# Kernel optimization log

Hardware: AMD Instinct MI355X
Metric: run time of the kernel (lower is better)

The kernel has to match this reference:

```python
import jax, jax.numpy as jnp
import numpy as np

B, C, H, W = 32, 64, 56, 56
REPN, NK, SMALL = 50, 17, 3   # repN=64-int(64*0.23), nk=ceil(51/3)
GROUPS = 4                     # N_rep
EPS = 1e-5


def _build_index_mats():
    """Reduce the fallback's python scatter-add loops to exact linear maps.
    For flat position p=r*NK+j the roll shifts depend only on p%3, so each
    shift class s gets a (REPN,NK) count matrix over source nk-slots."""
    rng = np.random.RandomState(123)
    ghost = np.sort(rng.choice(C, C - REPN, replace=False))
    rep = np.array(sorted(set(range(C)) - set(ghost.tolist())), np.int32)
    Mh = np.zeros((3, REPN, NK), np.int32)
    Mv = np.zeros((3, REPN, NK), np.int32)
    Mid = np.zeros((REPN, NK), np.int32)
    for _ in range(GROUPS):
        for r in range(REPN):
            perm = rng.permutation(NK)
            for p in range(NK):
                Mh[(r * NK + p) % 3, r, perm[p]] += 1
        for r in range(REPN):
            perm = rng.permutation(NK)
            for p in range(NK):
                Mv[(r * NK + p) % 3, r, perm[p]] += 1
        kk = rng.randint(0, NK, REPN)
        for r in range(REPN):
            Mid[r, kk[r]] += 1
    return ghost.astype(np.int32), rep, Mh, Mv, Mid


def setup_inputs() -> dict:
    key = jax.random.key(0)
    k1, k2, k3 = jax.random.split(key, 3)
    ghost, rep, Mh, Mv, Mid = _build_index_mats()
    return {
        "inputs": jax.random.normal(k1, (B, C, H, W), jnp.float32),
        "w0": jax.random.normal(k2, (REPN * NK, 1, SMALL, SMALL), jnp.float32) * 0.1,
        "w1": jax.random.normal(k3, (REPN * NK, 1, SMALL, SMALL), jnp.float32) * 0.1,
        "Mh": jnp.asarray(Mh), "Mv": jnp.asarray(Mv), "Mid": jnp.asarray(Mid),
        "ghost_idx": jnp.asarray(ghost), "rep_idx": jnp.asarray(rep),
    }


def _bn(x):
    # BatchNorm2d in training mode, affine weight=1 / bias=0 (init values)
    m = x.mean(axis=(0, 2, 3), keepdims=True)
    v = x.var(axis=(0, 2, 3), keepdims=True)
    return (x - m) / jnp.sqrt(v + EPS)


def reference(inputs, w0, w1, Mh, Mv, Mid, ghost_idx, rep_idx):
    rep_in = inputs[:, rep_idx]      # (B, REPN, H, W)
    ghost_in = inputs[:, ghost_idx]  # (B, ghostN, H, W)

    def conv(w):  # depthwise-grouped conv: groups=REPN, each 1->NK channels
        return jax.lax.conv_general_dilated(
            rep_in, w, window_strides=(1, 1), padding=((2, 2), (2, 2)),
            dimension_numbers=('NCHW', 'OIHW', 'NCHW'),
            feature_group_count=REPN)

    out = conv(w0) + conv(w1)                       # (B, REPN*NK, H+2, W+2)
    xv = out.reshape(B, REPN, NK, H + 2, W + 2)

    Mhf, Mvf, Midf = (m.astype(xv.dtype) for m in (Mh, Mv, Mid))
    sh1, sw1 = (0, 1, 2), (0, 2, 1)   # lora1: shifts (i%3, 2i%3)
    sh2, sw2 = (0, 2, 1), (0, 1, 2)   # lora2: shifts (2i%3, i%3)

    lora1 = sum(jnp.roll(jnp.einsum('rk,brkhw->brhw', Mhf[s], xv),
                         (sh1[s], sw1[s]), axis=(2, 3)) for s in range(3))
    lora2 = sum(jnp.roll(jnp.einsum('rk,brkhw->brhw', Mvf[s], xv),
                         (sh2[s], sw2[s]), axis=(2, 3)) for s in range(3))
    small = jnp.einsum('rk,brkhw->brhw', Midf, xv)

    # center-crop back to (H, W): dh = dw = 1
    lora1 = lora1[:, :, 1:1 + H, 1:1 + W]
    lora2 = lora2[:, :, 1:1 + H, 1:1 + W]
    small = small[:, :, 1:1 + H, 1:1 + W]

    x = _bn(lora1) + _bn(lora2) + _bn(small) + rep_in
    return jnp.concatenate([x, ghost_in], axis=1)   # (B, C, H, W)
```

## Files before the change

kernel.cpp:

```cpp
#include <hip/hip_runtime.h>
#include <hip/hip_cooperative_groups.h>

namespace cg = cooperative_groups;

#define Bn 32
#define Cn 64
#define Hn 56
#define Wn 56
#define REPN 50
#define NKn 17
#define HWn (Hn*Wn)
#define NSTATf 100352.0f
#define EPSf 1e-5f

#define PART_OFF 0
#define WEFF_OFF 9600
#define WEFF_N   (REPN*72)

#define SEGH 7
#define NTASK 112
#define GRID_FUSED 2048

__device__ __forceinline__ void weff_one(int idx,
        const float* __restrict__ w0, const float* __restrict__ w1,
        const int* __restrict__ Mh, const int* __restrict__ Mv,
        const int* __restrict__ Mid, float* __restrict__ ws)
{
    int r   = idx / 72;
    int rem = idx % 72;
    int ij  = rem >> 3;
    int t   = rem & 7;
    if (t == 7) { ws[WEFF_OFF + idx] = 0.f; return; }
    const int* M = (t < 3) ? (Mh + (t*REPN + r)*NKn)
                 : (t < 6) ? (Mv + ((t-3)*REPN + r)*NKn)
                           : (Mid + r*NKn);
    float acc = 0.f;
    #pragma unroll
    for (int k = 0; k < NKn; ++k)
        acc += (float)M[k] * (w0[(r*NKn + k)*9 + ij] + w1[(r*NKn + k)*9 + ij]);
    ws[WEFF_OFF + idx] = acc;
}

__global__ void k_weff(const float* __restrict__ w0, const float* __restrict__ w1,
                       const int* __restrict__ Mh, const int* __restrict__ Mv,
                       const int* __restrict__ Mid, float* __restrict__ ws)
{
    int idx = blockIdx.x * blockDim.x + threadIdx.x;
    if (idx < WEFF_N) weff_one(idx, w0, w1, Mh, Mv, Mid, ws);
}

__device__ __forceinline__ void load_row8c(const float* __restrict__ ch, int row, int q,
                                           float* __restrict__ X, float& c55)
{
    bool rv = (row >= 0) && (row < Hn);
    int rc = rv ? row : 0;
    const float* rp = ch + rc*Wn;
    float4 c0 = *(const float4*)(rp + (q ? 4*q - 4 : 0));
    float4 c1 = *(const float4*)(rp + 4*q);
    int ox = (4*q + 4 <= 55) ? 4*q + 4 : 55;
    float cx = rp[ox];
    float mr = rv ? 1.f : 0.f;
    float m0 = (rv && q > 0)  ? 1.f : 0.f;
    float mx = (rv && q < 13) ? 1.f : 0.f;
    X[0]=c0.y*m0; X[1]=c0.z*m0; X[2]=c0.w*m0;
    X[3]=c1.x*mr; X[4]=c1.y*mr; X[5]=c1.z*mr; X[6]=c1.w*mr;
    X[7]=cx*mx;
    c55 = (q == 0) ? rp[55]*mr : 0.f;
}

template <typename F>
__device__ __forceinline__ void conv_walk(const float* __restrict__ ch,
        const float* __restrict__ swk, int tid, F emit)
{
    if (tid >= NTASK) return;
    int seg = tid / 14;
    int q   = tid - seg*14;
    int h0  = seg * SEGH;
    bool top = (seg == 0);

    float W[5][8], C[5], T[8];
    {
        float dummy;
        if (top) load_row8c(ch, 55, q, T, dummy);
    }
    #pragma unroll
    for (int k = 0; k < 5; ++k)
        load_row8c(ch, h0 - 3 + k, q, W[k], C[k]);

    #pragma unroll
    for (int s = 0; s < SEGH; ++s) {
        int h = h0 + s;
        float Wn8[8], Cn1;
        load_row8c(ch, h + 2, q, Wn8, Cn1);

        int z = 0;
        asm volatile("" : "+v"(z));
        const float* wz = swk + z;

        float l1[4], l2[4], sm[4];
        #pragma unroll
        for (int p = 0; p < 4; ++p) { l1[p]=0.f; l2[p]=0.f; sm[p]=0.f; }
        #pragma unroll
        for (int i = 0; i < 3; ++i)
            #pragma unroll
            for (int j = 0; j < 3; ++j) {
                int ij = i*3 + j;
                float4 wa = *(const float4*)(wz + ij*8);
                float4 wb = *(const float4*)(wz + ij*8 + 4);
                float wh0 = wa.x, wh1 = wa.y, wh2 = wa.z, wv0 = wa.w;
                float wv1 = wb.x, wv2 = wb.y, wid = wb.z;
                #pragma unroll
                for (int p = 0; p < 4; ++p) {
                    float a  = W[2+i][p+2+j];
                    l1[p] = fmaf(a, wh0, l1[p]);
                    l2[p] = fmaf(a, wv0, l2[p]);
                    sm[p] = fmaf(a, wid, sm[p]);
                    float bA = W[1+i][p+j];
                    l1[p] = fmaf(bA, wh1, l1[p]);
                    l2[p] = fmaf(bA, wv2, l2[p]);
                    float bB = W[i][p+1+j];
                    l1[p] = fmaf(bB, wh2, l1[p]);
                    l2[p] = fmaf(bB, wv1, l2[p]);
                }
            }
        if (q == 0) {
            #pragma unroll
            for (int i = 0; i < 3; ++i) {
                l1[0] = fmaf(C[1+i], wz[(3*i)*8 + 1], l1[0]);
                l2[0] = fmaf(C[1+i], wz[(3*i)*8 + 5], l2[0]);
            }
        }
        if (s == 0 && top) {
            #pragma unroll
            for (int j = 0; j < 3; ++j)
                #pragma unroll
                for (int p = 0; p < 4; ++p) {
                    l1[p] = fmaf(T[p+1+j], wz[j*8 + 2], l1[p]);
                    l2[p] = fmaf(T[p+1+j], wz[j*8 + 4], l2[p]);
                }
        }
        float res[4] = {W[3][3], W[3][4], W[3][5], W[3][6]};
        emit(h, q, l1, l2, sm, res);

        #pragma unroll
        for (int k = 0; k < 4; ++k) {
            #pragma unroll
            for (int x = 0; x < 8; ++x) W[k][x] = W[k+1][x];
            C[k] = C[k+1];
        }
        #pragma unroll
        for (int x = 0; x < 8; ++x) W[4][x] = Wn8[x];
        C[4] = Cn1;
    }
}

__global__ void __launch_bounds__(128, 2) k_fused(const float* __restrict__ in,
        const float* __restrict__ w0, const float* __restrict__ w1,
        const int* __restrict__ Mh, const int* __restrict__ Mv,
        const int* __restrict__ Mid,
        const int* __restrict__ rep_idx, const int* __restrict__ ghost_idx,
        float* __restrict__ ws, float* __restrict__ out)
{
    cg::grid_group grid = cg::this_grid();
    int tid = threadIdx.x;
    int v = blockIdx.x;
    int c = v & 63;
    int b = v >> 6;
    bool ghost = (c >= REPN);

    __shared__ float swk[72];
    __shared__ float red[2][6];
    __shared__ float sred[6];

    {
        int gidx = blockIdx.x * 128 + tid;
        if (gidx < WEFF_N) weff_one(gidx, w0, w1, Mh, Mv, Mid, ws);
    }
    if (ghost) {
        int cin = ghost_idx[c - REPN];
        const float4* s4 = (const float4*)(in + ((size_t)(b*Cn + cin))*HWn);
        float4* d4 = (float4*)(out + ((size_t)(b*Cn + c))*HWn);
        for (int i = tid; i < HWn/4; i += 128) d4[i] = s4[i];
    }
    grid.sync();

    if (!ghost) {
        int r = c;
        if (tid < 72) swk[tid] = ws[WEFF_OFF + r*72 + tid];
        __syncthreads();
        const float* ch = in + ((size_t)(b*Cn + rep_idx[r]))*HWn;

        float s1=0.f,q1=0.f,s2=0.f,q2=0.f,s3=0.f,q3=0.f;
        conv_walk(ch, swk, tid,
            [&](int h, int q, float* l1, float* l2, float* sm, float* res) {
                (void)h; (void)q; (void)res;
                #pragma unroll
                for (int p = 0; p < 4; ++p) {
                    s1 += l1[p]; q1 += l1[p]*l1[p];
                    s2 += l2[p]; q2 += l2[p]*l2[p];
                    s3 += sm[p]; q3 += sm[p]*sm[p];
                }
            });
        {
            float vals[6] = {s1,q1,s2,q2,s3,q3};
            int lane = tid & 63, wave = tid >> 6;
            #pragma unroll
            for (int x = 0; x < 6; ++x) {
                float y = vals[x];
                for (int o = 32; o; o >>= 1) y += __shfl_down(y, o, 64);
                if (lane == 0) red[wave][x] = y;
            }
        }
        __syncthreads();
        if (tid < 6)
            ws[PART_OFF + (tid*REPN + c)*Bn + b] = red[0][tid] + red[1][tid];
    }
    grid.sync();

    if (ghost) return;
    int r = c;
    if (tid < 6) {
        const float* pp = ws + PART_OFF + (tid*REPN + r)*Bn;
        float s = 0.f;
        #pragma unroll
        for (int i = 0; i < Bn; ++i) s += pp[i];
        sred[tid] = s;
    }
    __syncthreads();
    const float inv = 1.0f / NSTATf;
    float m1 = sred[0]*inv, v1 = sred[1]*inv - m1*m1;
    float m2 = sred[2]*inv, v2 = sred[3]*inv - m2*m2;
    float m3 = sred[4]*inv, v3 = sred[5]*inv - m3*m3;
    float r1 = rsqrtf(v1 + EPSf), r2 = rsqrtf(v2 + EPSf), r3 = rsqrtf(v3 + EPSf);

    const float* ch = in + ((size_t)(b*Cn + rep_idx[r]))*HWn;
    float* dst = out + ((size_t)(b*Cn + c))*HWn;

    conv_walk(ch, swk, tid,
        [&](int h, int q, float* l1, float* l2, float* sm, float* res) {
            float4 o;
            o.x = (l1[0]-m1)*r1 + (l2[0]-m2)*r2 + (sm[0]-m3)*r3 + res[0];
            o.y = (l1[1]-m1)*r1 + (l2[1]-m2)*r2 + (sm[1]-m3)*r3 + res[1];
            o.z = (l1[2]-m1)*r1 + (l2[2]-m2)*r2 + (sm[2]-m3)*r3 + res[2];
            o.w = (l1[3]-m1)*r1 + (l2[3]-m2)*r2 + (sm[3]-m3)*r3 + res[3];
            *(float4*)(dst + h*Wn + 4*q) = o;
        });
}

__global__ void __launch_bounds__(128) k_stats(const float* __restrict__ in,
        const int* __restrict__ rep_idx, float* __restrict__ ws)
{
    int bid = blockIdx.x;
    int r = bid % REPN;
    int b = bid / REPN;
    int tid = threadIdx.x;

    __shared__ float swk[72];
    if (tid < 72) swk[tid] = ws[WEFF_OFF + r*72 + tid];
    __syncthreads();
    const float* ch = in + ((size_t)(b*Cn + rep_idx[r]))*HWn;

    float s1=0.f,q1=0.f,s2=0.f,q2=0.f,s3=0.f,q3=0.f;
    conv_walk(ch, swk, tid,
        [&](int h, int q, float* l1, float* l2, float* sm, float* res) {
            (void)h; (void)q; (void)res;
            #pragma unroll
            for (int p = 0; p < 4; ++p) {
                s1 += l1[p]; q1 += l1[p]*l1[p];
                s2 += l2[p]; q2 += l2[p]*l2[p];
                s3 += sm[p]; q3 += sm[p]*sm[p];
            }
        });

    __shared__ float red[2][6];
    float vals[6] = {s1,q1,s2,q2,s3,q3};
    int lane = tid & 63, wave = tid >> 6;
    #pragma unroll
    for (int v = 0; v < 6; ++v) {
        float x = vals[v];
        for (int o = 32; o; o >>= 1) x += __shfl_down(x, o, 64);
        if (lane == 0) red[wave][v] = x;
    }
    __syncthreads();
    if (tid < 6)
        ws[PART_OFF + (tid*REPN + r)*Bn + b] = red[0][tid] + red[1][tid];
}

__global__ void __launch_bounds__(128) k_out(const float* __restrict__ in,
        const int* __restrict__ rep_idx, const int* __restrict__ ghost_idx,
        const float* __restrict__ ws, float* __restrict__ out)
{
    int bid = blockIdx.x;
    int c = bid % Cn;
    int b = bid / Cn;
    int tid = threadIdx.x;

    if (c >= REPN) {
        int cin = ghost_idx[c - REPN];
        const float4* s4 = (const float4*)(in + ((size_t)(b*Cn + cin))*HWn);
        float4* d4 = (float4*)(out + ((size_t)(b*Cn + c))*HWn);
        for (int i = tid; i < HWn/4; i += 128) d4[i] = s4[i];
        return;
    }

    int r = c;
    __shared__ float swk[72];
    __shared__ float sred[6];
    if (tid < 72) swk[tid] = ws[WEFF_OFF + r*72 + tid];
    if (tid < 6) {
        const float* pp = ws + PART_OFF + (tid*REPN + r)*Bn;
        float s = 0.f;
        #pragma unroll
        for (int i = 0; i < Bn; ++i) s += pp[i];
        sred[tid] = s;
    }
    __syncthreads();
    const float inv = 1.0f / NSTATf;
    float m1 = sred[0]*inv, v1 = sred[1]*inv - m1*m1;
    float m2 = sred[2]*inv, v2 = sred[3]*inv - m2*m2;
    float m3 = sred[4]*inv, v3 = sred[5]*inv - m3*m3;
    float r1 = rsqrtf(v1 + EPSf), r2 = rsqrtf(v2 + EPSf), r3 = rsqrtf(v3 + EPSf);

    const float* ch = in + ((size_t)(b*Cn + rep_idx[r]))*HWn;
    float* dst = out + ((size_t)(b*Cn + c))*HWn;

    conv_walk(ch, swk, tid,
        [&](int h, int q, float* l1, float* l2, float* sm, float* res) {
            float4 o;
            o.x = (l1[0]-m1)*r1 + (l2[0]-m2)*r2 + (sm[0]-m3)*r3 + res[0];
            o.y = (l1[1]-m1)*r1 + (l2[1]-m2)*r2 + (sm[1]-m3)*r3 + res[1];
            o.z = (l1[2]-m1)*r1 + (l2[2]-m2)*r2 + (sm[2]-m3)*r3 + res[2];
            o.w = (l1[3]-m1)*r1 + (l2[3]-m2)*r2 + (sm[3]-m3)*r3 + res[3];
            *(float4*)(dst + h*Wn + 4*q) = o;
        });
}

extern "C" void kernel_launch(void* const* d_in, const int* in_sizes, int n_in,
                              void* d_out, int out_size, void* d_ws, size_t ws_size,
                              hipStream_t stream) {
    const float* in   = (const float*)d_in[0];
    const float* w0   = (const float*)d_in[1];
    const float* w1   = (const float*)d_in[2];
    const int*   Mh   = (const int*)d_in[3];
    const int*   Mv   = (const int*)d_in[4];
    const int*   Mid  = (const int*)d_in[5];
    const int*   ghost= (const int*)d_in[6];
    const int*   rep  = (const int*)d_in[7];
    float* out  = (float*)d_out;
    float* ws   = (float*)d_ws;

    int maxBlk = 0;
    hipError_t qerr = hipOccupancyMaxActiveBlocksPerMultiprocessor(
        &maxBlk, (const void*)k_fused, 128, 0);
    bool coop_ok = (qerr == hipSuccess) && (maxBlk >= 8);

    if (coop_ok) {
        void* args[] = { (void*)&in, (void*)&w0, (void*)&w1, (void*)&Mh,
                         (void*)&Mv, (void*)&Mid, (void*)&rep, (void*)&ghost,
                         (void*)&ws, (void*)&out };
        hipError_t lerr = hipLaunchCooperativeKernel((const void*)k_fused,
                              dim3(GRID_FUSED), dim3(128), args, 0, stream);
        if (lerr == hipSuccess) return;
    }
    k_weff<<<(WEFF_N + 127)/128, 128, 0, stream>>>(w0, w1, Mh, Mv, Mid, ws);
    k_stats<<<Bn*REPN, 128, 0, stream>>>(in, rep, ws);
    k_out<<<Bn*Cn, 128, 0, stream>>>(in, rep, ghost, ws, out);
}
```

Before: 134.8 us.

## Replace cooperative grid syncs with per-channel atomic counters and local weight folding

Replaces the cooperative launch and its two grid-wide barriers with an ordinary launch plus a small init kernel. Each block folds its own effective 3x3 weights into shared memory instead of writing them to global memory first. BatchNorm statistics are now accumulated with atomics, and each channel's 32 batch blocks spin on a counter, so blocks wait only for their own channel rather than the whole grid. This removes the cost of full grid synchronisation, but it depends on all blocks of a channel being co-resident (otherwise it can deadlock), makes the float sums order-nondeterministic, and adds an extra kernel launch.

```diff
diff --git a/kernel.cpp b/kernel.cpp
--- a/kernel.cpp
+++ b/kernel.cpp
@@ -1,7 +1,4 @@
 #include <hip/hip_runtime.h>
-#include <hip/hip_cooperative_groups.h>
-
-namespace cg = cooperative_groups;
 
 #define Bn 32
 #define Cn 64
@@ -13,13 +10,16 @@
 #define NSTATf 100352.0f
 #define EPSf 1e-5f
 
-#define PART_OFF 0
-#define WEFF_OFF 9600
+#define GSUM_OFF 0
+#define GCNT_OFF 512
+#define INIT_N   2112
+#define PART_OFF 4096
+#define WEFF_OFF (4096+9600)
 #define WEFF_N   (REPN*72)
 
 #define SEGH 7
 #define NTASK 112
-#define GRID_FUSED 2048
+#define GRID_MONO 2048
 
 __device__ __forceinline__ void weff_one(int idx,
         const float* __restrict__ w0, const float* __restrict__ w1,
@@ -47,6 +47,11 @@
 {
     int idx = blockIdx.x * blockDim.x + threadIdx.x;
     if (idx < WEFF_N) weff_one(idx, w0, w1, Mh, Mv, Mid, ws);
+}
+
+__global__ void k_init(float* __restrict__ ws)
+{
+    for (int i = threadIdx.x; i < INIT_N; i += 256) ws[i] = 0.f;
 }
 
 __device__ __forceinline__ void load_row8c(const float* __restrict__ ch, int row, int q,
@@ -154,86 +159,94 @@
     }
 }
 
-__global__ void __launch_bounds__(128, 2) k_fused(const float* __restrict__ in,
+__global__ void __launch_bounds__(128, 2) k_mono(const float* __restrict__ in,
         const float* __restrict__ w0, const float* __restrict__ w1,
         const int* __restrict__ Mh, const int* __restrict__ Mv,
         const int* __restrict__ Mid,
         const int* __restrict__ rep_idx, const int* __restrict__ ghost_idx,
         float* __restrict__ ws, float* __restrict__ out)
 {
-    cg::grid_group grid = cg::this_grid();
     int tid = threadIdx.x;
     int v = blockIdx.x;
     int c = v & 63;
     int b = v >> 6;
-    bool ghost = (c >= REPN);
-
-    __shared__ float swk[72];
-    __shared__ float red[2][6];
-    __shared__ float sred[6];
-
-    {
-        int gidx = blockIdx.x * 128 + tid;
-        if (gidx < WEFF_N) weff_one(gidx, w0, w1, Mh, Mv, Mid, ws);
-    }
-    if (ghost) {
+
+    if (c >= REPN) {
         int cin = ghost_idx[c - REPN];
         const float4* s4 = (const float4*)(in + ((size_t)(b*Cn + cin))*HWn);
         float4* d4 = (float4*)(out + ((size_t)(b*Cn + c))*HWn);
         for (int i = tid; i < HWn/4; i += 128) d4[i] = s4[i];
-    }
-    grid.sync();
-
-    if (!ghost) {
-        int r = c;
-        if (tid < 72) swk[tid] = ws[WEFF_OFF + r*72 + tid];
-        __syncthreads();
-        const float* ch = in + ((size_t)(b*Cn + rep_idx[r]))*HWn;
-
-        float s1=0.f,q1=0.f,s2=0.f,q2=0.f,s3=0.f,q3=0.f;
-        conv_walk(ch, swk, tid,
-            [&](int h, int q, float* l1, float* l2, float* sm, float* res) {
-                (void)h; (void)q; (void)res;
-                #pragma unroll
-                for (int p = 0; p < 4; ++p) {
-                    s1 += l1[p]; q1 += l1[p]*l1[p];
-                    s2 += l2[p]; q2 += l2[p]*l2[p];
-                    s3 += sm[p]; q3 += sm[p]*sm[p];
-                }
-            });
-        {
-            float vals[6] = {s1,q1,s2,q2,s3,q3};
-            int lane = tid & 63, wave = tid >> 6;
-            #pragma unroll
-            for (int x = 0; x < 6; ++x) {
-                float y = vals[x];
-                for (int o = 32; o; o >>= 1) y += __shfl_down(y, o, 64);
-                if (lane == 0) red[wave][x] = y;
+        return;
+    }
+    int r = c;
+
+    __shared__ float swk[72];
+    __shared__ float red[2][6];
+    __shared__ float sred[6];
+
+    if (tid < 72) {
+        int ij = tid >> 3, tt = tid & 7;
+        if (tt == 7) swk[tid] = 0.f;
+        else {
+            const int* M = (tt < 3) ? (Mh + (tt*REPN + r)*NKn)
+                         : (tt < 6) ? (Mv + ((tt-3)*REPN + r)*NKn)
+                                    : (Mid + r*NKn);
+            float acc = 0.f;
+            #pragma unroll
+            for (int k = 0; k < NKn; ++k)
+                acc += (float)M[k] * (w0[(r*NKn + k)*9 + ij] + w1[(r*NKn + k)*9 + ij]);
+            swk[tid] = acc;
+        }
+    }
+    __syncthreads();
+
+    const float* ch = in + ((size_t)(b*Cn + rep_idx[r]))*HWn;
+
+    float s1=0.f,q1=0.f,s2=0.f,q2=0.f,s3=0.f,q3=0.f;
+    conv_walk(ch, swk, tid,
+        [&](int h, int q, float* l1, float* l2, float* sm, float* res) {
+            (void)h; (void)q; (void)res;
+            #pragma unroll
+            for (int p = 0; p < 4; ++p) {
+                s1 += l1[p]; q1 += l1[p]*l1[p];
+                s2 += l2[p]; q2 += l2[p]*l2[p];
+                s3 += sm[p]; q3 += sm[p]*sm[p];
             }
-        }
-        __syncthreads();
-        if (tid < 6)
-            ws[PART_OFF + (tid*REPN + c)*Bn + b] = red[0][tid] + red[1][tid];
-    }
-    grid.sync();
-
-    if (ghost) return;
-    int r = c;
+        });
+    {
+        float vals[6] = {s1,q1,s2,q2,s3,q3};
+        int lane = tid & 63, wave = tid >> 6;
+        #pragma unroll
+        for (int x = 0; x < 6; ++x) {
+            float y = vals[x];
+            for (int o = 32; o; o >>= 1) y += __shfl_down(y, o, 64);
+            if (lane == 0) red[wave][x] = y;
+        }
+    }
+    __syncthreads();
+
+    float* gsum = ws + GSUM_OFF + r*8;
+    unsigned* gcnt = ((unsigned*)ws) + GCNT_OFF + r*32;
     if (tid < 6) {
-        const float* pp = ws + PART_OFF + (tid*REPN + r)*Bn;
-        float s = 0.f;
-        #pragma unroll
-        for (int i = 0; i < Bn; ++i) s += pp[i];
-        sred[tid] = s;
-    }
-    __syncthreads();
+        atomicAdd(&gsum[tid], red[0][tid] + red[1][tid]);
+        __threadfence();
+    }
+    __syncthreads();
+    if (tid == 0) {
+        atomicAdd(gcnt, 1u);
+        while (atomicAdd(gcnt, 0u) < (unsigned)Bn)
+            __builtin_amdgcn_s_sleep(2);
+    }
+    __syncthreads();
+    if (tid < 6) sred[tid] = atomicAdd(&gsum[tid], 0.f);
+    __syncthreads();
+
     const float inv = 1.0f / NSTATf;
     float m1 = sred[0]*inv, v1 = sred[1]*inv - m1*m1;
     float m2 = sred[2]*inv, v2 = sred[3]*inv - m2*m2;
     float m3 = sred[4]*inv, v3 = sred[5]*inv - m3*m3;
     float r1 = rsqrtf(v1 + EPSf), r2 = rsqrtf(v2 + EPSf), r3 = rsqrtf(v3 + EPSf);
 
-    const float* ch = in + ((size_t)(b*Cn + rep_idx[r]))*HWn;
     float* dst = out + ((size_t)(b*Cn + c))*HWn;
 
     conv_walk(ch, swk, tid,
@@ -351,16 +364,14 @@
 
     int maxBlk = 0;
     hipError_t qerr = hipOccupancyMaxActiveBlocksPerMultiprocessor(
-        &maxBlk, (const void*)k_fused, 128, 0);
-    bool coop_ok = (qerr == hipSuccess) && (maxBlk >= 8);
-
-    if (coop_ok) {
-        void* args[] = { (void*)&in, (void*)&w0, (void*)&w1, (void*)&Mh,
-                         (void*)&Mv, (void*)&Mid, (void*)&rep, (void*)&ghost,
-                         (void*)&ws, (void*)&out };
-        hipError_t lerr = hipLaunchCooperativeKernel((const void*)k_fused,
-                              dim3(GRID_FUSED), dim3(128), args, 0, stream);
-        if (lerr == hipSuccess) return;
+        &maxBlk, (const void*)k_mono, 128, 0);
+    bool mono_ok = (qerr == hipSuccess) && (maxBlk >= 8);
+
+    if (mono_ok) {
+        k_init<<<1, 256, 0, stream>>>(ws);
+        k_mono<<<GRID_MONO, 128, 0, stream>>>(in, w0, w1, Mh, Mv, Mid,
+                                              rep, ghost, ws, out);
+        return;
     }
     k_weff<<<(WEFF_N + 127)/128, 128, 0, stream>>>(w0, w1, Mh, Mv, Mid, ws);
     k_stats<<<Bn*REPN, 128, 0, stream>>>(in, rep, ws);
```

Result: no change. 134.4 us (-0.3%).
